# Performance work log

Measured on AMD Instinct MI355X. Metric: run time of the kernel, lower is better.

The kernel has to match this reference:

```python
import jax, jax.numpy as jnp
import numpy as np

NUP, NDOWN, NMO, NCONF, NSAMP = 16, 16, 64, 128, 2048


def setup_inputs() -> dict:
    key = jax.random.key(0)
    x = jax.random.normal(key, (NSAMP, NUP + NDOWN, NMO), dtype=jnp.float32)
    # Configurations: each config selects NUP (resp. NDOWN) DISTINCT orbitals out of NMO
    # (distinctness keeps the Slater matrices nonsingular, as in real CI expansions).
    rng = np.random.default_rng(0)
    cup = np.stack([np.sort(rng.choice(NMO, NUP, replace=False)) for _ in range(NCONF)]).astype(np.int32)
    cdn = np.stack([np.sort(rng.choice(NMO, NDOWN, replace=False)) for _ in range(NCONF)]).astype(np.int32)
    return {
        "input": x,
        "configs_up": jnp.asarray(cup),
        "configs_down": jnp.asarray(cdn),
    }


def reference(input, configs_up, configs_down):
    # input: [S, NUP+NDOWN, NMO]; configs_*: [C, NUP] int
    mo_up = input[:, :NUP, :]    # [S, NUP, NMO]
    mo_dn = input[:, NUP:, :]    # [S, NDOWN, NMO]
    # Gather orbital columns for every configuration in one shot.
    # take along orbital axis -> [S, n_elec, C, n_elec]; move config axis forward.
    up = jnp.transpose(jnp.take(mo_up, configs_up, axis=2), (0, 2, 1, 3))   # [S, C, NUP, NUP]
    dn = jnp.transpose(jnp.take(mo_dn, configs_down, axis=2), (0, 2, 1, 3))  # [S, C, NDOWN, NDOWN]
    # Batched determinants and spin-product -> [S, C]
    return jnp.linalg.det(up) * jnp.linalg.det(dn)
```

## Files before the change

kernel.cpp:

```cpp
#include <hip/hip_runtime.h>

#define NSAMP 2048
#define NCONF 128
#define NMO   64
#define NE    16

__global__ __launch_bounds__(256, 1)
void SlaterPooling_45543833207162_kernel(const float* __restrict__ x,
                                         const int*   __restrict__ cup,
                                         const int*   __restrict__ cdn,
                                         float*       __restrict__ out) {
  __shared__ float tile[4 * 64 * NE];
  float4* tile4 = reinterpret_cast<float4*>(tile);

  {
    const float4* src = reinterpret_cast<const float4*>(
        x + (size_t)blockIdx.x * 2 * (2 * NE * NMO));
#pragma unroll
    for (int k = 0; k < 4; ++k) {
      const int   f4 = threadIdx.x + k * 256;
      const float4 v = src[f4];
      const int flat  = f4 * 4;
      const int plane = flat >> 10;
      const int r     = (flat >> 6) & 15;
      const int c4    = (flat >> 2) & 15;
      const int rlo = r & 3, rhi = r >> 2;
      const float vv[4] = {v.x, v.y, v.z, v.w};
#pragma unroll
      for (int d = 0; d < 4; ++d) {
        const int cc = 4 * c4 + d;
        const int h  = (d ^ c4) & 3;
        tile[plane * 1024 + cc * NE + (((rhi ^ h) << 2) | rlo)] = vv[d];
      }
    }
  }
  __syncthreads();

  const int s_local = threadIdx.x >> 7;
  const int c       = threadIdx.x & 127;
  float result = 1.0f;

#pragma unroll 1
  for (int spin = 0; spin < 2; ++spin) {
    const int4* cfg4 = reinterpret_cast<const int4*>(
        (spin ? cdn : cup) + c * NE);
    const int4 q0 = cfg4[0], q1 = cfg4[1], q2 = cfg4[2], q3 = cfg4[3];
    const int cidx[16] = {q0.x, q0.y, q0.z, q0.w,  q1.x, q1.y, q1.z, q1.w,
                          q2.x, q2.y, q2.z, q2.w,  q3.x, q3.y, q3.z, q3.w};

    const float4* plane4 = tile4 + (s_local * 2 + spin) * 256;

    float L[NE - 1][NE];
    float det = 1.0f;

#pragma unroll
    for (int j = 0; j < NE; ++j) {
      const int cj = cidx[j];
      const int h  = (cj ^ (cj >> 2)) & 3;
      const float4* col = plane4 + cj * 4;
      float a[NE];
      { const float4 t = col[0 ^ h]; a[ 0]=t.x; a[ 1]=t.y; a[ 2]=t.z; a[ 3]=t.w; }
      { const float4 t = col[1 ^ h]; a[ 4]=t.x; a[ 5]=t.y; a[ 6]=t.z; a[ 7]=t.w; }
      { const float4 t = col[2 ^ h]; a[ 8]=t.x; a[ 9]=t.y; a[10]=t.z; a[11]=t.w; }
      { const float4 t = col[3 ^ h]; a[12]=t.x; a[13]=t.y; a[14]=t.z; a[15]=t.w; }

#pragma unroll
      for (int k = 0; k < NE - 1; ++k) {
        if (k < j) {
          const float uk = a[k];
#pragma unroll
          for (int i = k + 1; i < NE; ++i)
            a[i] = fmaf(-L[k][i], uk, a[i]);
        }
      }

      const float p = a[j];
      det *= p;
      if (j < NE - 1) {
        float r = __builtin_amdgcn_rcpf(p);
        r = r * fmaf(-p, r, 2.0f);
#pragma unroll
        for (int i = j + 1; i < NE; ++i)
          L[j][i] = a[i] * r;
      }
    }
    result *= det;
  }

  out[(blockIdx.x * 2 + s_local) * NCONF + c] = result;
}

extern "C" void kernel_launch(void* const* d_in, const int* in_sizes, int n_in,
                              void* d_out, int out_size, void* d_ws, size_t ws_size,
                              hipStream_t stream) {
  const float* x   = (const float*)d_in[0];
  const int*   cup = (const int*)d_in[1];
  const int*   cdn = (const int*)d_in[2];
  float*       out = (float*)d_out;

  dim3 grid(NSAMP / 2), block(256);
  hipLaunchKernelGGL(SlaterPooling_45543833207162_kernel, grid, block, 0, stream,
                     x, cup, cdn, out);
}
```

Before: 27.98 us.

## Process LU columns in pairs with packed float2 FMAs

Restructures the left-looking LU elimination to handle two columns per step and store the multipliers as float2 vectors. The updates can then map to packed FP32 FMA instructions (v_pk_fma_f32) on CDNA3/4, cutting the VALU instruction count. The price is some redundant work on even/odd boundaries, since row k is updated from pair index k>>1, plus the risk of extra register pressure or shuffles for the broadcast scalars.

Result: slower. 29.53 us (+5.5%).

```diff
diff --git a/kernel.cpp b/kernel.cpp
--- a/kernel.cpp
+++ b/kernel.cpp
@@ -4,6 +4,8 @@
 #define NCONF 128
 #define NMO   64
 #define NE    16
+
+typedef float v2f __attribute__((ext_vector_type(2)));
 
 __global__ __launch_bounds__(256, 1)
 void SlaterPooling_45543833207162_kernel(const float* __restrict__ x,
@@ -50,38 +52,71 @@
 
     const float4* plane4 = tile4 + (s_local * 2 + spin) * 256;
 
-    float L[NE - 1][NE];
+    v2f L2[NE - 2][8];
     float det = 1.0f;
 
 #pragma unroll
-    for (int j = 0; j < NE; ++j) {
-      const int cj = cidx[j];
-      const int h  = (cj ^ (cj >> 2)) & 3;
-      const float4* col = plane4 + cj * 4;
-      float a[NE];
-      { const float4 t = col[0 ^ h]; a[ 0]=t.x; a[ 1]=t.y; a[ 2]=t.z; a[ 3]=t.w; }
-      { const float4 t = col[1 ^ h]; a[ 4]=t.x; a[ 5]=t.y; a[ 6]=t.z; a[ 7]=t.w; }
-      { const float4 t = col[2 ^ h]; a[ 8]=t.x; a[ 9]=t.y; a[10]=t.z; a[11]=t.w; }
-      { const float4 t = col[3 ^ h]; a[12]=t.x; a[13]=t.y; a[14]=t.z; a[15]=t.w; }
+    for (int t = 0; t < 8; ++t) {
+      const int j0 = 2 * t, j1 = 2 * t + 1;
+
+      v2f a2[8], b2[8];
+      {
+        const int cj = cidx[j0];
+        const int h  = (cj ^ (cj >> 2)) & 3;
+        const float4* col = plane4 + cj * 4;
+        { const float4 v = col[0 ^ h]; a2[0] = v2f{v.x, v.y}; a2[1] = v2f{v.z, v.w}; }
+        { const float4 v = col[1 ^ h]; a2[2] = v2f{v.x, v.y}; a2[3] = v2f{v.z, v.w}; }
+        { const float4 v = col[2 ^ h]; a2[4] = v2f{v.x, v.y}; a2[5] = v2f{v.z, v.w}; }
+        { const float4 v = col[3 ^ h]; a2[6] = v2f{v.x, v.y}; a2[7] = v2f{v.z, v.w}; }
+      }
+      {
+        const int cj = cidx[j1];
+        const int h  = (cj ^ (cj >> 2)) & 3;
+        const float4* col = plane4 + cj * 4;
+        { const float4 v = col[0 ^ h]; b2[0] = v2f{v.x, v.y}; b2[1] = v2f{v.z, v.w}; }
+        { const float4 v = col[1 ^ h]; b2[2] = v2f{v.x, v.y}; b2[3] = v2f{v.z, v.w}; }
+        { const float4 v = col[2 ^ h]; b2[4] = v2f{v.x, v.y}; b2[5] = v2f{v.z, v.w}; }
+        { const float4 v = col[3 ^ h]; b2[6] = v2f{v.x, v.y}; b2[7] = v2f{v.z, v.w}; }
+      }
 
 #pragma unroll
-      for (int k = 0; k < NE - 1; ++k) {
-        if (k < j) {
-          const float uk = a[k];
+      for (int k = 0; k < NE - 2; ++k) {
+        if (k < j0) {
+          const float ua = (k & 1) ? a2[k >> 1].y : a2[k >> 1].x;
+          const float ub = (k & 1) ? b2[k >> 1].y : b2[k >> 1].x;
+          const v2f uav = {ua, ua};
+          const v2f ubv = {ub, ub};
 #pragma unroll
-          for (int i = k + 1; i < NE; ++i)
-            a[i] = fmaf(-L[k][i], uk, a[i]);
+          for (int m = k >> 1; m < 8; ++m) {
+            const v2f l = L2[k][m];
+            a2[m] = __builtin_elementwise_fma(-l, uav, a2[m]);
+            b2[m] = __builtin_elementwise_fma(-l, ubv, b2[m]);
+          }
         }
       }
 
-      const float p = a[j];
-      det *= p;
-      if (j < NE - 1) {
-        float r = __builtin_amdgcn_rcpf(p);
-        r = r * fmaf(-p, r, 2.0f);
+      const float p0 = a2[t].x;
+      det *= p0;
+      float r0 = __builtin_amdgcn_rcpf(p0);
+      r0 = r0 * fmaf(-p0, r0, 2.0f);
+      const v2f r0v = {r0, r0};
+      const float ub0 = b2[t].x;
+      const v2f w0v = {r0 * ub0, r0 * ub0};
 #pragma unroll
-        for (int i = j + 1; i < NE; ++i)
-          L[j][i] = a[i] * r;
+      for (int m = t; m < 8; ++m) {
+        if (t < 7) L2[j0][m] = a2[m] * r0v;
+        b2[m] = __builtin_elementwise_fma(-a2[m], w0v, b2[m]);
+      }
+
+      const float p1 = b2[t].y;
+      det *= p1;
+      if (t < 7) {
+        float r1 = __builtin_amdgcn_rcpf(p1);
+        r1 = r1 * fmaf(-p1, r1, 2.0f);
+        const v2f r1v = {r1, r1};
+#pragma unroll
+        for (int m = t; m < 8; ++m)
+          L2[j1][m] = b2[m] * r1v;
       }
     }
     result *= det;
```
